# Optimization experiments

Hardware: AMD Instinct MI355X
Metric: run time of the kernel (lower is better)

Reference implementation:

```python
import jax, jax.numpy as jnp
import numpy as np

N1, N2, D = 8192, 8192, 128

def setup_inputs() -> dict:
    key = jax.random.key(0)
    k1, k2 = jax.random.split(key)
    desc1 = jax.random.normal(k1, (N1, D), dtype=jnp.float32)
    desc2 = jax.random.normal(k2, (N2, D), dtype=jnp.float32)
    return {"desc1": desc1, "desc2": desc2}

def reference(desc1, desc2):
    # sim: [N1, N2] descriptor similarity matrix
    sim = desc1 @ desc2.T
    # mutual nearest-neighbor matching ('nnm' mode)
    nn12 = jnp.argmax(sim, axis=1)            # [N1] best match in image 2 for each kp in image 1
    nn21 = jnp.argmax(sim, axis=0)            # [N2] best match in image 1 for each kp in image 2
    ids1 = jnp.arange(sim.shape[0])
    mutual = nn21[nn12] == ids1               # mutual-consistency check
    # dense jit-friendly encoding of the ragged match list: -1 where no mutual match
    matches0 = jnp.where(mutual, nn12, -1)    # [N1] int
    # matching_scores0 = top-1 similarity per row (torch.topk(..., k=1)[0].squeeze())
    scores = jnp.max(sim, axis=1)             # [N1]
    return matches0, scores
```

## Files before the change

### kernel.cpp

```cpp
#include <hip/hip_runtime.h>
#include <stdint.h>

#define N1 8192
#define N2 8192
#define DK 128
#define TAU 0.08f
#define BIAS 256.0f
#define LDR 132

typedef _Float16 half8 __attribute__((ext_vector_type(8)));
typedef _Float16 half4 __attribute__((ext_vector_type(4)));
typedef float floatx4 __attribute__((ext_vector_type(4)));

__device__ __align__(16) _Float16 g_Af[N1 * DK];
__device__ __align__(16) _Float16 g_Bf[N2 * DK];
__device__ __align__(16) float2 g_rowtop2[64 * N1];
__device__ __align__(16) float2 g_coltop2[64 * N2];
__device__ int g_nn12[N1];
__device__ int g_nn21[N2];

__device__ __forceinline__ float bval(float key) {
    return __uint_as_float(__float_as_uint(key) & 0xFFFFFF80u);
}
__device__ __forceinline__ int bidx(float key) {
    return (int)(__float_as_uint(key) & 127u);
}
__device__ __forceinline__ void push2f(float& t1, float& t2, float p) {
    float m = __builtin_amdgcn_fmed3f(t1, t2, p);
    t1 = fmaxf(t1, p);
    t2 = m;
}
__device__ __forceinline__ void merge2f(float& t1, float& t2, float o1, float o2) {
    float x = fmaxf(t2, o2);
    float m = __builtin_amdgcn_fmed3f(t1, o1, x);
    t1 = fmaxf(t1, o1);
    t2 = m;
}
__device__ __forceinline__ float2 m2(float2 a, float2 b) {
    merge2f(a.x, a.y, b.x, b.y);
    return a;
}
#define DPPF(x, ctrl) __int_as_float(__builtin_amdgcn_update_dpp( \
        0, __float_as_int(x), (ctrl), 0xF, 0xF, true))

__device__ __forceinline__ unsigned mono32(float v) {
    unsigned u = __float_as_uint(v);
    return u ^ ((u & 0x80000000u) ? 0xFFFFFFFFu : 0x80000000u);
}
__device__ __forceinline__ float unmono32(unsigned k) {
    unsigned u = (k & 0x80000000u) ? (k ^ 0x80000000u) : ~k;
    return __uint_as_float(u);
}
__device__ __forceinline__ unsigned long long pack64(float d, unsigned idx) {
    return ((unsigned long long)mono32(d) << 32) | (unsigned)(~idx);
}

__global__ __launch_bounds__(256) void convert_kernel(const float* __restrict__ A,
                                                      const float* __restrict__ B) {
    int t = blockIdx.x * blockDim.x + threadIdx.x;
    const int perMat = N1 * (DK / 4);
    int which = (t >= perMat) ? 1 : 0;
    const float* src = which ? B : A;
    _Float16* dst = which ? g_Bf : g_Af;
    int i = which ? t - perMat : t;
    int m = i >> 5;
    int kq = i & 31;
    float4 v = *reinterpret_cast<const float4*>(src + (size_t)m * DK + kq * 4);
    half4 h = {(_Float16)v.x, (_Float16)v.y, (_Float16)v.z, (_Float16)v.w};
    *reinterpret_cast<half4*>(dst + (size_t)m * DK + kq * 4) = h;
}

__global__ __launch_bounds__(256) void simf16_kernel() {
    __shared__ union {
        _Float16 Bs[128 * LDR];
        float2 scr[128][34];
    } sm;
    __shared__ float2 lmerge[2][128];

    const int tid  = threadIdx.x;
    const int lane = tid & 63;
    const int wave = tid >> 6;
    const int wm = wave >> 1, wn = wave & 1;
    const int fr = lane & 15, q = lane >> 4;

    const int flat = blockIdx.y * 64 + blockIdx.x;
    const int xcd = flat & 7;
    const int j = flat >> 3;
    const int ty = j >> 3;
    const int tx = ((j & 7) << 3) | xcd;
    const int row0 = ty * 128, col0 = tx * 128;

    float4 breg[8];
#pragma unroll
    for (int i = 0; i < 8; ++i) {
        int f = i * 256 + tid;
        int r = f >> 4, c = f & 15;
        breg[i] = *reinterpret_cast<const float4*>(g_Bf + (size_t)(col0 + r) * DK + c * 8);
    }

    const _Float16* Abase = g_Af + (size_t)(row0 + wm * 64 + fr) * DK + q * 8;

    half8 af[4], afn[4];
#pragma unroll
    for (int mt = 0; mt < 4; ++mt)
        af[mt] = *reinterpret_cast<const half8*>(Abase + mt * 16 * DK);

    floatx4 acc[4][4];
#pragma unroll
    for (int mt = 0; mt < 4; ++mt)
#pragma unroll
        for (int nt = 0; nt < 4; ++nt)
            acc[mt][nt] = (floatx4){0.f, 0.f, 0.f, 0.f};

#pragma unroll
    for (int i = 0; i < 8; ++i) {
        int f = i * 256 + tid;
        int r = f >> 4, c = f & 15;
        *reinterpret_cast<float4*>(&sm.Bs[r * LDR + c * 8]) = breg[i];
    }

    __syncthreads();

#pragma unroll
    for (int ks = 0; ks < 4; ++ks) {
        if (ks < 3) {
#pragma unroll
            for (int mt = 0; mt < 4; ++mt)
                afn[mt] = *reinterpret_cast<const half8*>(Abase + mt * 16 * DK + (ks + 1) * 32);
        }
        half8 bf[4];
#pragma unroll
        for (int nt = 0; nt < 4; ++nt)
            bf[nt] = *reinterpret_cast<const half8*>(&sm.Bs[(wn * 64 + nt * 16 + fr) * LDR + ks * 32 + q * 8]);
#pragma unroll
        for (int mt = 0; mt < 4; ++mt)
#pragma unroll
            for (int nt = 0; nt < 4; ++nt)
                acc[mt][nt] = __builtin_amdgcn_mfma_f32_16x16x32_f16(af[mt], bf[nt], acc[mt][nt], 0, 0, 0);
        if (ks < 3) {
#pragma unroll
            for (int mt = 0; mt < 4; ++mt)
                af[mt] = afn[mt];
        }
    }

#pragma unroll
    for (int mt = 0; mt < 4; ++mt)
#pragma unroll
        for (int nt = 0; nt < 4; ++nt)
#pragma unroll
            for (int reg = 0; reg < 4; ++reg)
                acc[mt][nt][reg] = __uint_as_float(
                    __float_as_uint(acc[mt][nt][reg] + BIAS) & 0xFFFFFF80u);

    __syncthreads();

#pragma unroll
    for (int mt = 0; mt < 4; ++mt) {
#pragma unroll
        for (int reg = 0; reg < 4; ++reg) {
            float t1 = 0.f, t2 = 0.f;
#pragma unroll
            for (int nt = 0; nt < 4; ++nt)
                push2f(t1, t2, __uint_as_float(__float_as_uint(acc[mt][nt][reg])
                                               | (unsigned)(wn * 64 + nt * 16 + fr)));
            sm.scr[wm * 64 + mt * 16 + q * 4 + reg][wn * 16 + fr] = make_float2(t1, t2);
        }
    }
    __syncthreads();

    {
        const int row = tid >> 1, h = tid & 1;
        const float4* p = reinterpret_cast<const float4*>(&sm.scr[row][h * 16]);
        float4 v0 = p[0], v1 = p[1], v2 = p[2], v3 = p[3];
        float4 v4 = p[4], v5 = p[5], v6 = p[6], v7 = p[7];
        float2 r0 = m2(make_float2(v0.x, v0.y), make_float2(v0.z, v0.w));
        float2 r1 = m2(make_float2(v1.x, v1.y), make_float2(v1.z, v1.w));
        float2 r2 = m2(make_float2(v2.x, v2.y), make_float2(v2.z, v2.w));
        float2 r3 = m2(make_float2(v3.x, v3.y), make_float2(v3.z, v3.w));
        float2 r4 = m2(make_float2(v4.x, v4.y), make_float2(v4.z, v4.w));
        float2 r5 = m2(make_float2(v5.x, v5.y), make_float2(v5.z, v5.w));
        float2 r6 = m2(make_float2(v6.x, v6.y), make_float2(v6.z, v6.w));
        float2 r7 = m2(make_float2(v7.x, v7.y), make_float2(v7.z, v7.w));
        r0 = m2(r0, r1); r2 = m2(r2, r3); r4 = m2(r4, r5); r6 = m2(r6, r7);
        r0 = m2(r0, r2); r4 = m2(r4, r6);
        r0 = m2(r0, r4);
        float o1 = __shfl_xor(r0.x, 1, 64), o2 = __shfl_xor(r0.y, 1, 64);
        merge2f(r0.x, r0.y, o1, o2);
        if (h == 0) g_rowtop2[(size_t)tx * N1 + row0 + row] = r0;
    }

#pragma unroll
    for (int nt = 0; nt < 4; ++nt) {
        float t1 = 0.f, t2 = 0.f;
#pragma unroll
        for (int mt = 0; mt < 4; ++mt)
#pragma unroll
            for (int reg = 0; reg < 4; ++reg)
                push2f(t1, t2, __uint_as_float(__float_as_uint(acc[mt][nt][reg])
                                               | (unsigned)(wm * 64 + mt * 16 + q * 4 + reg)));
        float o1 = __shfl_xor(t1, 16, 64), o2 = __shfl_xor(t2, 16, 64);
        merge2f(t1, t2, o1, o2);
        o1 = __shfl_xor(t1, 32, 64); o2 = __shfl_xor(t2, 32, 64);
        merge2f(t1, t2, o1, o2);
        if (q == 0) lmerge[wm][wn * 64 + nt * 16 + fr] = make_float2(t1, t2);
    }
    __syncthreads();
    if (tid < 128) {
        float2 a = lmerge[0][tid], b = lmerge[1][tid];
        merge2f(a.x, a.y, b.x, b.y);
        g_coltop2[(size_t)ty * N2 + col0 + tid] = a;
    }
}

__global__ __launch_bounds__(256) void fix_kernel(const float* __restrict__ A,
                                                  const float* __restrict__ B,
                                                  float* __restrict__ out) {
    __shared__ float2 tile[64 * 16];
    __shared__ unsigned long long slot[16];
    __shared__ int cand[256];
    __shared__ int cand_cnt;

    const int tid = threadIdx.x;
    const bool rowside = blockIdx.x >= 512;
    const int base0 = (blockIdx.x & 511) * 16;
    const float2* top2 = rowside ? g_rowtop2 : g_coltop2;

#pragma unroll
    for (int i = 0; i < 4; ++i) {
        int idx = i * 256 + tid;
        int grp = idx >> 4, c = idx & 15;
        tile[grp * 16 + c] = top2[(size_t)grp * N1 + base0 + c];
    }
    if (tid < 16) slot[tid] = 0ULL;
    if (tid == 0) cand_cnt = 0;
    __syncthreads();

    const int c = tid >> 4, j = tid & 15;
    float mx = 0.f;
#pragma unroll
    for (int s = 0; s < 4; ++s)
        mx = fmaxf(mx, tile[(j * 4 + s) * 16 + c].x);
    mx = fmaxf(mx, DPPF(mx, 0xB1));
    mx = fmaxf(mx, DPPF(mx, 0x4E));
    mx = fmaxf(mx, DPPF(mx, 0x124));
    mx = fmaxf(mx, DPPF(mx, 0x128));
    const float thr = bval(mx) - TAU;
#pragma unroll
    for (int s = 0; s < 4; ++s) {
        int grp = j * 4 + s;
        float2 e = tile[grp * 16 + c];
        if (bval(e.x) >= thr) {
            int o = grp * 128 + bidx(e.x);
            int si = atomicAdd(&cand_cnt, 1);
            if (si < 256) cand[si] = (c << 16) | o;
        }
        if (bval(e.y) >= thr) {
            int o = grp * 128 + bidx(e.y);
            int si = atomicAdd(&cand_cnt, 1);
            if (si < 256) cand[si] = (c << 16) | o;
        }
    }
    __syncthreads();

    const int nc = min(cand_cnt, 256);
    for (int i = tid; i < nc; i += 256) {
        int pc = cand[i];
        int cl = pc >> 16, other = pc & 0xFFFF;
        const float* ar = rowside ? (A + (size_t)(base0 + cl) * DK) : (A + (size_t)other * DK);
        const float* br = rowside ? (B + (size_t)other * DK) : (B + (size_t)(base0 + cl) * DK);
        float d = 0.0f;
#pragma unroll
        for (int k4 = 0; k4 < DK / 4; ++k4) {
            float4 a = *reinterpret_cast<const float4*>(ar + k4 * 4);
            float4 b = *reinterpret_cast<const float4*>(br + k4 * 4);
            d = fmaf(a.x, b.x, d);
            d = fmaf(a.y, b.y, d);
            d = fmaf(a.z, b.z, d);
            d = fmaf(a.w, b.w, d);
        }
        atomicMax(&slot[cl], pack64(d, (unsigned)other));
    }
    __syncthreads();

    if (tid < 16) {
        unsigned long long p = slot[tid];
        int idx = base0 + tid;
        if (rowside) {
            g_nn12[idx] = (int)(~(unsigned)p);
            out[N1 + idx] = unmono32((unsigned)(p >> 32));
        } else {
            g_nn21[idx] = (int)(~(unsigned)p);
        }
    }
}

__global__ __launch_bounds__(256) void mutual_kernel(float* __restrict__ out) {
    int i = blockIdx.x * blockDim.x + threadIdx.x;
    if (i < N1) {
        int m = g_nn12[i];
        out[i] = (float)((g_nn21[m] == i) ? m : -1);
    }
}

extern "C" void kernel_launch(void* const* d_in, const int* in_sizes, int n_in,
                              void* d_out, int out_size, void* d_ws, size_t ws_size,
                              hipStream_t stream) {
    const float* A = (const float*)d_in[0];
    const float* B = (const float*)d_in[1];
    float* out = (float*)d_out;

    convert_kernel<<<2 * N1 * (DK / 4) / 256, 256, 0, stream>>>(A, B);
    dim3 grid(64, 64);
    simf16_kernel<<<grid, 256, 0, stream>>>();
    fix_kernel<<<1024, 256, 0, stream>>>(A, B, out);
    mutual_kernel<<<N1 / 256, 256, 0, stream>>>(out);
}
```

Before: 121.7 us.

## Process two column tiles per block with prefetched B and MFMA priority hints

Each block of the similarity kernel now handles two 128x128 column tiles in a loop instead of one, and the grid is halved to match. The second B tile is loaded from global memory into registers while the first tile's epilogue reductions run. The column-max and row-max epilogues are reordered so the column merge happens before the row scratch pass, and s_setprio raises wave priority around the MFMA block. The aim is to hide B-load latency and amortize block launch overhead, at the cost of more register pressure and fewer blocks to balance across CUs.

```diff
diff --git a/kernel.cpp b/kernel.cpp
--- a/kernel.cpp
+++ b/kernel.cpp
@@ -86,130 +86,154 @@
     const int flat = blockIdx.y * 64 + blockIdx.x;
     const int xcd = flat & 7;
     const int j = flat >> 3;
-    const int ty = j >> 3;
-    const int tx = ((j & 7) << 3) | xcd;
-    const int row0 = ty * 128, col0 = tx * 128;
+    const int ty = j >> 2;
+    const int h = j & 3;
+    const int row0 = ty * 128;
+
+    const _Float16* Abase = g_Af + (size_t)(row0 + wm * 64 + fr) * DK + q * 8;
 
     float4 breg[8];
-#pragma unroll
-    for (int i = 0; i < 8; ++i) {
-        int f = i * 256 + tid;
-        int r = f >> 4, c = f & 15;
-        breg[i] = *reinterpret_cast<const float4*>(g_Bf + (size_t)(col0 + r) * DK + c * 8);
-    }
-
-    const _Float16* Abase = g_Af + (size_t)(row0 + wm * 64 + fr) * DK + q * 8;
-
-    half8 af[4], afn[4];
-#pragma unroll
-    for (int mt = 0; mt < 4; ++mt)
-        af[mt] = *reinterpret_cast<const half8*>(Abase + mt * 16 * DK);
-
-    floatx4 acc[4][4];
-#pragma unroll
-    for (int mt = 0; mt < 4; ++mt)
-#pragma unroll
-        for (int nt = 0; nt < 4; ++nt)
-            acc[mt][nt] = (floatx4){0.f, 0.f, 0.f, 0.f};
-
-#pragma unroll
-    for (int i = 0; i < 8; ++i) {
-        int f = i * 256 + tid;
-        int r = f >> 4, c = f & 15;
-        *reinterpret_cast<float4*>(&sm.Bs[r * LDR + c * 8]) = breg[i];
-    }
-
-    __syncthreads();
-
-#pragma unroll
-    for (int ks = 0; ks < 4; ++ks) {
-        if (ks < 3) {
+    {
+        const int tx = ((2 * h) << 3) | xcd;
+        const _Float16* gB = g_Bf + (size_t)(tx * 128) * DK;
+#pragma unroll
+        for (int i = 0; i < 8; ++i) {
+            int f = i * 256 + tid;
+            int r = f >> 4, c = f & 15;
+            breg[i] = *reinterpret_cast<const float4*>(gB + (size_t)r * DK + c * 8);
+        }
+    }
+
+#pragma unroll
+    for (int t = 0; t < 2; ++t) {
+        const int tx = ((2 * h + t) << 3) | xcd;
+        const int col0 = tx * 128;
+
+#pragma unroll
+        for (int i = 0; i < 8; ++i) {
+            int f = i * 256 + tid;
+            int r = f >> 4, c = f & 15;
+            *reinterpret_cast<float4*>(&sm.Bs[r * LDR + c * 8]) = breg[i];
+        }
+
+        floatx4 acc[4][4];
+#pragma unroll
+        for (int mt = 0; mt < 4; ++mt)
+#pragma unroll
+            for (int nt = 0; nt < 4; ++nt)
+                acc[mt][nt] = (floatx4){0.f, 0.f, 0.f, 0.f};
+
+        half8 af[4], afn[4];
+#pragma unroll
+        for (int mt = 0; mt < 4; ++mt)
+            af[mt] = *reinterpret_cast<const half8*>(Abase + mt * 16 * DK);
+
+        __syncthreads();
+
+#pragma unroll
+        for (int ks = 0; ks < 4; ++ks) {
+            if (ks < 3) {
+#pragma unroll
+                for (int mt = 0; mt < 4; ++mt)
+                    afn[mt] = *reinterpret_cast<const half8*>(Abase + mt * 16 * DK + (ks + 1) * 32);
+            }
+            half8 bf[4];
+#pragma unroll
+            for (int nt = 0; nt < 4; ++nt)
+                bf[nt] = *reinterpret_cast<const half8*>(&sm.Bs[(wn * 64 + nt * 16 + fr) * LDR + ks * 32 + q * 8]);
+            __builtin_amdgcn_s_setprio(1);
 #pragma unroll
             for (int mt = 0; mt < 4; ++mt)
-                afn[mt] = *reinterpret_cast<const half8*>(Abase + mt * 16 * DK + (ks + 1) * 32);
-        }
-        half8 bf[4];
-#pragma unroll
-        for (int nt = 0; nt < 4; ++nt)
-            bf[nt] = *reinterpret_cast<const half8*>(&sm.Bs[(wn * 64 + nt * 16 + fr) * LDR + ks * 32 + q * 8]);
+#pragma unroll
+                for (int nt = 0; nt < 4; ++nt)
+                    acc[mt][nt] = __builtin_amdgcn_mfma_f32_16x16x32_f16(af[mt], bf[nt], acc[mt][nt], 0, 0, 0);
+            __builtin_amdgcn_s_setprio(0);
+            if (ks < 3) {
+#pragma unroll
+                for (int mt = 0; mt < 4; ++mt)
+                    af[mt] = afn[mt];
+            }
+        }
+
 #pragma unroll
         for (int mt = 0; mt < 4; ++mt)
 #pragma unroll
             for (int nt = 0; nt < 4; ++nt)
-                acc[mt][nt] = __builtin_amdgcn_mfma_f32_16x16x32_f16(af[mt], bf[nt], acc[mt][nt], 0, 0, 0);
-        if (ks < 3) {
+#pragma unroll
+                for (int reg = 0; reg < 4; ++reg)
+                    acc[mt][nt][reg] = __uint_as_float(
+                        __float_as_uint(acc[mt][nt][reg] + BIAS) & 0xFFFFFF80u);
+
+#pragma unroll
+        for (int nt = 0; nt < 4; ++nt) {
+            float t1 = 0.f, t2 = 0.f;
 #pragma unroll
             for (int mt = 0; mt < 4; ++mt)
-                af[mt] = afn[mt];
-        }
-    }
-
-#pragma unroll
-    for (int mt = 0; mt < 4; ++mt)
-#pragma unroll
-        for (int nt = 0; nt < 4; ++nt)
-#pragma unroll
-            for (int reg = 0; reg < 4; ++reg)
-                acc[mt][nt][reg] = __uint_as_float(
-                    __float_as_uint(acc[mt][nt][reg] + BIAS) & 0xFFFFFF80u);
-
-    __syncthreads();
-
-#pragma unroll
-    for (int mt = 0; mt < 4; ++mt) {
-#pragma unroll
-        for (int reg = 0; reg < 4; ++reg) {
-            float t1 = 0.f, t2 = 0.f;
-#pragma unroll
-            for (int nt = 0; nt < 4; ++nt)
-                push2f(t1, t2, __uint_as_float(__float_as_uint(acc[mt][nt][reg])
-                                               | (unsigned)(wn * 64 + nt * 16 + fr)));
-            sm.scr[wm * 64 + mt * 16 + q * 4 + reg][wn * 16 + fr] = make_float2(t1, t2);
-        }
-    }
-    __syncthreads();
-
-    {
-        const int row = tid >> 1, h = tid & 1;
-        const float4* p = reinterpret_cast<const float4*>(&sm.scr[row][h * 16]);
-        float4 v0 = p[0], v1 = p[1], v2 = p[2], v3 = p[3];
-        float4 v4 = p[4], v5 = p[5], v6 = p[6], v7 = p[7];
-        float2 r0 = m2(make_float2(v0.x, v0.y), make_float2(v0.z, v0.w));
-        float2 r1 = m2(make_float2(v1.x, v1.y), make_float2(v1.z, v1.w));
-        float2 r2 = m2(make_float2(v2.x, v2.y), make_float2(v2.z, v2.w));
-        float2 r3 = m2(make_float2(v3.x, v3.y), make_float2(v3.z, v3.w));
-        float2 r4 = m2(make_float2(v4.x, v4.y), make_float2(v4.z, v4.w));
-        float2 r5 = m2(make_float2(v5.x, v5.y), make_float2(v5.z, v5.w));
-        float2 r6 = m2(make_float2(v6.x, v6.y), make_float2(v6.z, v6.w));
-        float2 r7 = m2(make_float2(v7.x, v7.y), make_float2(v7.z, v7.w));
-        r0 = m2(r0, r1); r2 = m2(r2, r3); r4 = m2(r4, r5); r6 = m2(r6, r7);
-        r0 = m2(r0, r2); r4 = m2(r4, r6);
-        r0 = m2(r0, r4);
-        float o1 = __shfl_xor(r0.x, 1, 64), o2 = __shfl_xor(r0.y, 1, 64);
-        merge2f(r0.x, r0.y, o1, o2);
-        if (h == 0) g_rowtop2[(size_t)tx * N1 + row0 + row] = r0;
-    }
-
-#pragma unroll
-    for (int nt = 0; nt < 4; ++nt) {
-        float t1 = 0.f, t2 = 0.f;
-#pragma unroll
-        for (int mt = 0; mt < 4; ++mt)
-#pragma unroll
-            for (int reg = 0; reg < 4; ++reg)
-                push2f(t1, t2, __uint_as_float(__float_as_uint(acc[mt][nt][reg])
-                                               | (unsigned)(wm * 64 + mt * 16 + q * 4 + reg)));
-        float o1 = __shfl_xor(t1, 16, 64), o2 = __shfl_xor(t2, 16, 64);
-        merge2f(t1, t2, o1, o2);
-        o1 = __shfl_xor(t1, 32, 64); o2 = __shfl_xor(t2, 32, 64);
-        merge2f(t1, t2, o1, o2);
-        if (q == 0) lmerge[wm][wn * 64 + nt * 16 + fr] = make_float2(t1, t2);
-    }
-    __syncthreads();
-    if (tid < 128) {
-        float2 a = lmerge[0][tid], b = lmerge[1][tid];
-        merge2f(a.x, a.y, b.x, b.y);
-        g_coltop2[(size_t)ty * N2 + col0 + tid] = a;
+#pragma unroll
+                for (int reg = 0; reg < 4; ++reg)
+                    push2f(t1, t2, __uint_as_float(__float_as_uint(acc[mt][nt][reg])
+                                                   | (unsigned)(wm * 64 + mt * 16 + q * 4 + reg)));
+            float o1 = __shfl_xor(t1, 16, 64), o2 = __shfl_xor(t2, 16, 64);
+            merge2f(t1, t2, o1, o2);
+            o1 = __shfl_xor(t1, 32, 64); o2 = __shfl_xor(t2, 32, 64);
+            merge2f(t1, t2, o1, o2);
+            if (q == 0) lmerge[wm][wn * 64 + nt * 16 + fr] = make_float2(t1, t2);
+        }
+
+        __syncthreads();
+
+#pragma unroll
+        for (int mt = 0; mt < 4; ++mt) {
+#pragma unroll
+            for (int reg = 0; reg < 4; ++reg) {
+                float t1 = 0.f, t2 = 0.f;
+#pragma unroll
+                for (int nt = 0; nt < 4; ++nt)
+                    push2f(t1, t2, __uint_as_float(__float_as_uint(acc[mt][nt][reg])
+                                                   | (unsigned)(wn * 64 + nt * 16 + fr)));
+                sm.scr[wm * 64 + mt * 16 + q * 4 + reg][wn * 16 + fr] = make_float2(t1, t2);
+            }
+        }
+
+        if (t == 0) {
+            const _Float16* gB = g_Bf + (size_t)((((2 * h + 1) << 3) | xcd) * 128) * DK;
+#pragma unroll
+            for (int i = 0; i < 8; ++i) {
+                int f = i * 256 + tid;
+                int r = f >> 4, c = f & 15;
+                breg[i] = *reinterpret_cast<const float4*>(gB + (size_t)r * DK + c * 8);
+            }
+        }
+
+        if (tid < 128) {
+            float2 a = lmerge[0][tid], b = lmerge[1][tid];
+            merge2f(a.x, a.y, b.x, b.y);
+            g_coltop2[(size_t)ty * N2 + col0 + tid] = a;
+        }
+        __syncthreads();
+
+        {
+            const int row = tid >> 1, hh = tid & 1;
+            const float4* p = reinterpret_cast<const float4*>(&sm.scr[row][hh * 16]);
+            float4 v0 = p[0], v1 = p[1], v2 = p[2], v3 = p[3];
+            float4 v4 = p[4], v5 = p[5], v6 = p[6], v7 = p[7];
+            float2 r0 = m2(make_float2(v0.x, v0.y), make_float2(v0.z, v0.w));
+            float2 r1 = m2(make_float2(v1.x, v1.y), make_float2(v1.z, v1.w));
+            float2 r2 = m2(make_float2(v2.x, v2.y), make_float2(v2.z, v2.w));
+            float2 r3 = m2(make_float2(v3.x, v3.y), make_float2(v3.z, v3.w));
+            float2 r4 = m2(make_float2(v4.x, v4.y), make_float2(v4.z, v4.w));
+            float2 r5 = m2(make_float2(v5.x, v5.y), make_float2(v5.z, v5.w));
+            float2 r6 = m2(make_float2(v6.x, v6.y), make_float2(v6.z, v6.w));
+            float2 r7 = m2(make_float2(v7.x, v7.y), make_float2(v7.z, v7.w));
+            r0 = m2(r0, r1); r2 = m2(r2, r3); r4 = m2(r4, r5); r6 = m2(r6, r7);
+            r0 = m2(r0, r2); r4 = m2(r4, r6);
+            r0 = m2(r0, r4);
+            float o1 = __shfl_xor(r0.x, 1, 64), o2 = __shfl_xor(r0.y, 1, 64);
+            merge2f(r0.x, r0.y, o1, o2);
+            if (hh == 0) g_rowtop2[(size_t)tx * N1 + row0 + row] = r0;
+        }
+
+        if (t == 0) __syncthreads();
     }
 }
 
@@ -311,7 +335,7 @@
     float* out = (float*)d_out;
 
     convert_kernel<<<2 * N1 * (DK / 4) / 256, 256, 0, stream>>>(A, B);
-    dim3 grid(64, 64);
+    dim3 grid(64, 32);
     simf16_kernel<<<grid, 256, 0, stream>>>();
     fix_kernel<<<1024, 256, 0, stream>>>(A, B, out);
     mutual_kernel<<<N1 / 256, 256, 0, stream>>>(out);
```

After: 140.2 us. 1.15x slower.
